# Kernel optimization log

Measured on AMD Instinct MI355X. Metric: run time of the kernel, lower is better.

## Reference

```python
import jax, jax.numpy as jnp
import numpy as np


def setup_inputs() -> dict:
    key = jax.random.key(0)
    k1, k2, k3, k4 = jax.random.split(key, 4)
    B, C, H, W = 8, 64, 64, 64
    Ck = C // 8  # query/key channels
    x = jax.random.normal(k1, (B, C, H, W), dtype=jnp.float32)
    # 1x1 conv1d weights (bias=False); spectral norm only rescales the weight,
    # so plain matrices are math-equivalent at a given parameter value.
    wq = jax.random.normal(k2, (Ck, C), dtype=jnp.float32) * (1.0 / np.sqrt(C))
    wk = jax.random.normal(k3, (Ck, C), dtype=jnp.float32) * (1.0 / np.sqrt(C))
    wv = jax.random.normal(k4, (C, C), dtype=jnp.float32) * (1.0 / np.sqrt(C))
    gamma = jnp.array([0.5], dtype=jnp.float32)  # nonzero so attention path is exercised
    return {"x": x, "wq": wq, "wk": wk, "wv": wv, "gamma": gamma}


def reference(x, wq, wk, wv, gamma):
    B, C, H, W = x.shape
    xf = x.reshape(B, C, H * W)                      # [B, C, N]
    f = jnp.einsum('kc,bcn->bkn', wq, xf)            # [B, C/8, N]
    g = jnp.einsum('kc,bcn->bkn', wk, xf)            # [B, C/8, N]
    h = jnp.einsum('oc,bcn->bon', wv, xf)            # [B, C,   N]
    scores = jnp.einsum('bkn,bkm->bnm', f, g)        # f^T g, [B, N, N]
    beta = jax.nn.softmax(scores, axis=1)            # softmax over dim=1 (rows), as in torch
    o = jnp.einsum('bcn,bnm->bcm', h, beta)          # [B, C, N]
    out = gamma[0] * o + xf
    return out.reshape(B, C, H, W)
```

## Files before the change

### kernel.cpp

```cpp
#include <hip/hip_runtime.h>
#include <hip/hip_bf16.h>

typedef __bf16 bf16x8 __attribute__((ext_vector_type(8)));
typedef float f32x4 __attribute__((ext_vector_type(4)));
typedef float f32x16 __attribute__((ext_vector_type(16)));
typedef unsigned int uint2v __attribute__((ext_vector_type(2)));

#define MFMA16 __builtin_amdgcn_mfma_f32_16x16x32_bf16
#define MFMA32 __builtin_amdgcn_mfma_f32_32x32x16_bf16

__device__ __forceinline__ unsigned short f2b(float f) {
  unsigned int u = __float_as_uint(f);
  u += 0x7FFFu + ((u >> 16) & 1u);
  return (unsigned short)(u >> 16);
}

__device__ __forceinline__ float b2f(unsigned short s) {
  return __uint_as_float(((unsigned)s) << 16);
}

union U128 {
  uint4 u;
  unsigned short s[8];
  bf16x8 b;
};

union BPack {
  __hip_bfloat162 h2;
  unsigned u;
};

__device__ __forceinline__ unsigned packbf(float a, float b) {
  BPack p;
  p.h2 = __float22bfloat162_rn(make_float2(a, b));
  return p.u;
}

__global__ __launch_bounds__(256, 2) void proj_kernel(
    const float* __restrict__ x, const float* __restrict__ wq,
    const float* __restrict__ wk, const float* __restrict__ wv_w,
    unsigned short* __restrict__ f_t, unsigned short* __restrict__ g_t,
    unsigned short* __restrict__ h_out) {
  __shared__ unsigned short xT[64 * 64];
  __shared__ unsigned short wT[96 * 72];

  const int tid = (int)threadIdx.x;
  const int wvp = tid >> 6;
  const int lane = tid & 63;
  const int b = (int)blockIdx.x & 7;
  const int n0 = ((int)blockIdx.x >> 3) << 6;

  {
    const float* xb = x + ((size_t)b << 18) + n0 + lane;
    const int c0 = wvp * 16;
    float xv[16];
#pragma unroll
    for (int cc = 0; cc < 16; ++cc) xv[cc] = xb[(size_t)(c0 + cc) << 12];
#pragma unroll
    for (int p = 0; p < 4; ++p) {
      const int c = c0 + 4 * p;
      uint2 d;
      d.x = packbf(xv[4 * p + 0], xv[4 * p + 1]);
      d.y = packbf(xv[4 * p + 2], xv[4 * p + 3]);
      const int g = c >> 3;
      const int idx = lane * 64 + (((g ^ (lane & 7)) << 3) | (((c >> 2) & 1) << 2));
      *(uint2*)&xT[idx] = d;
    }
  }
#pragma unroll
  for (int i = 0; i < 20; ++i) {
    const int idx = i * 256 + tid;
    const float wval = (idx < 512) ? wq[idx] * 1.44269504f
                     : (idx < 1024) ? wk[idx - 512]
                                    : wv_w[idx - 1024];
    wT[(idx >> 6) * 72 + (idx & 63)] = f2b(wval);
  }
  __syncthreads();

  const int t = lane & 15, q = lane >> 4;
  const int nloc = wvp * 16 + t;
  U128 Bf[2];
#pragma unroll
  for (int kp = 0; kp < 2; ++kp) {
    const int g = kp * 4 + q;
    Bf[kp].u = *(const uint4*)&xT[nloc * 64 + ((g ^ (nloc & 7)) << 3)];
  }
  const int nabs = n0 + nloc;
#pragma unroll
  for (int rt = 0; rt < 5; ++rt) {
    f32x4 acc = {0.f, 0.f, 0.f, 0.f};
#pragma unroll
    for (int kp = 0; kp < 2; ++kp) {
      U128 Af;
      Af.u = *(const uint4*)&wT[(rt * 16 + t) * 72 + ((kp * 4 + q) << 3)];
      acc = MFMA16(Af.b, Bf[kp].b, acc, 0, 0, 0);
    }
#pragma unroll
    for (int reg = 0; reg < 4; ++reg) {
      const int r = rt * 16 + 4 * q + reg;
      const unsigned short v = f2b(acc[reg]);
      if (r < 8)
        f_t[((size_t)((b << 12) + nabs) << 3) + r] = v;
      else if (r < 16)
        g_t[((size_t)((b << 12) + nabs) << 3) + (r - 8)] = v;
      else
        h_out[((size_t)b << 18) + ((size_t)(nabs >> 3) << 9) +
              ((r - 16) << 3) + (nabs & 7)] = v;
    }
  }
}

__global__ __launch_bounds__(256, 4) void attn_kernel(
    const unsigned short* __restrict__ f_t, const unsigned short* __restrict__ g_t,
    const unsigned short* __restrict__ h, const float* __restrict__ x,
    const float* __restrict__ gamma, float* __restrict__ out) {
  __shared__ unsigned short Opart[4][32][66];
  __shared__ float lred[4][32];
  __shared__ float lsum[32];

  const int tid = (int)threadIdx.x;
  const int wave = tid >> 6;
  const int lane = tid & 63;
  const int ml = lane & 31;
  const int hh = lane >> 5;

  const int b = (int)blockIdx.x & 7;
  const int m32 = ((int)blockIdx.x >> 3) << 5;

  const unsigned short* fb = f_t + ((size_t)b << 15);
  const unsigned short* hb = h + ((size_t)b << 18);

  U128 G;
  G.u = make_uint4(0u, 0u, 0u, 0u);
  if (hh == 0) G.u = *(const uint4*)(g_t + ((size_t)((b << 12) + m32 + ml) << 3));

  f32x16 O0 = {}, O1 = {};
  float lp = 0.f;

  const int nbase = wave << 10;

  const unsigned short* fp = fb + ((size_t)(nbase + ml) << 3);
  const unsigned short* hp = hb + ((nbase >> 3) << 9) + (hh << 9) + (ml << 3);

  U128 F0, F1, Ha0[4], Ha1[4];
  F0.u = *(const uint4*)(fp);
  Ha0[0].u = *(const uint4*)(hp);
  Ha0[1].u = *(const uint4*)(hp + 256);
  Ha0[2].u = *(const uint4*)(hp + 1024);
  Ha0[3].u = *(const uint4*)(hp + 1280);

  auto body = [&](const U128& Fv, const U128* Hv) {
    const f32x16 z = {};
    f32x16 S = MFMA32(Fv.b, G.b, z, 0, 0, 0);
    float e[16];
#pragma unroll
    for (int r = 0; r < 16; ++r) e[r] = __builtin_amdgcn_exp2f(S[r]);
    lp += (((e[0] + e[1]) + (e[2] + e[3])) + ((e[4] + e[5]) + (e[6] + e[7]))) +
          (((e[8] + e[9]) + (e[10] + e[11])) + ((e[12] + e[13]) + (e[14] + e[15])));
#pragma unroll
    for (int kt = 0; kt < 2; ++kt) {
      const unsigned A0 = packbf(e[8 * kt + 0], e[8 * kt + 1]);
      const unsigned A1 = packbf(e[8 * kt + 2], e[8 * kt + 3]);
      const unsigned B0 = packbf(e[8 * kt + 4], e[8 * kt + 5]);
      const unsigned B1 = packbf(e[8 * kt + 6], e[8 * kt + 7]);
      const uint2v r0 = __builtin_amdgcn_permlane32_swap(A0, B0, false, false);
      const uint2v r1 = __builtin_amdgcn_permlane32_swap(A1, B1, false, false);
      U128 P;
      P.u.x = r0[0];
      P.u.y = r1[0];
      P.u.z = r0[1];
      P.u.w = r1[1];
      O0 = MFMA32(Hv[2 * kt + 0].b, P.b, O0, 0, 0, 0);
      O1 = MFMA32(Hv[2 * kt + 1].b, P.b, O1, 0, 0, 0);
    }
  };

#pragma unroll 1
  for (int it2 = 0; it2 < 15; ++it2) {
    F1.u = *(const uint4*)(fp + 256);
    Ha1[0].u = *(const uint4*)(hp + 2048);
    Ha1[1].u = *(const uint4*)(hp + 2304);
    Ha1[2].u = *(const uint4*)(hp + 3072);
    Ha1[3].u = *(const uint4*)(hp + 3328);
    body(F0, Ha0);
    F0.u = *(const uint4*)(fp + 512);
    Ha0[0].u = *(const uint4*)(hp + 4096);
    Ha0[1].u = *(const uint4*)(hp + 4352);
    Ha0[2].u = *(const uint4*)(hp + 5120);
    Ha0[3].u = *(const uint4*)(hp + 5376);
    body(F1, Ha1);
    fp += 512;
    hp += 4096;
  }
  F1.u = *(const uint4*)(fp + 256);
  Ha1[0].u = *(const uint4*)(hp + 2048);
  Ha1[1].u = *(const uint4*)(hp + 2304);
  Ha1[2].u = *(const uint4*)(hp + 3072);
  Ha1[3].u = *(const uint4*)(hp + 3328);
  body(F0, Ha0);
  body(F1, Ha1);

  lp += __shfl_xor(lp, 32, 64);
  if (hh == 0) lred[wave][ml] = lp;
#pragma unroll
  for (int r = 0; r < 8; ++r) {
    const int c0 = ((2 * r) & 3) + 8 * (r >> 1) + 4 * hh;
    *(unsigned*)&Opart[wave][ml][c0] = packbf(O0[2 * r], O0[2 * r + 1]);
    *(unsigned*)&Opart[wave][ml][c0 + 32] = packbf(O1[2 * r], O1[2 * r + 1]);
  }
  __syncthreads();
  if (tid < 32)
    lsum[tid] = (lred[0][tid] + lred[1][tid]) + (lred[2][tid] + lred[3][tid]);
  __syncthreads();

  const int c = tid >> 2;
  const int m0l = (tid & 3) << 3;
  const float gam = gamma[0];
  float a[8];
#pragma unroll
  for (int j = 0; j < 8; ++j) a[j] = 0.f;
#pragma unroll
  for (int w = 0; w < 4; ++w)
#pragma unroll
    for (int j = 0; j < 8; ++j) a[j] += b2f(Opart[w][m0l + j][c]);

  const f32x4 l0 = *(const f32x4*)&lsum[m0l];
  const f32x4 l1 = *(const f32x4*)&lsum[m0l + 4];
  const size_t oi = (((size_t)b * 64 + c) << 12) + m32 + m0l;
  f32x4 xo0 = *(const f32x4*)(x + oi);
  f32x4 xo1 = *(const f32x4*)(x + oi + 4);
#pragma unroll
  for (int j = 0; j < 4; ++j) {
    xo0[j] += gam / l0[j] * a[j];
    xo1[j] += gam / l1[j] * a[j + 4];
  }
  *(f32x4*)(out + oi) = xo0;
  *(f32x4*)(out + oi + 4) = xo1;
}

extern "C" void kernel_launch(void* const* d_in, const int* in_sizes, int n_in,
                              void* d_out, int out_size, void* d_ws, size_t ws_size,
                              hipStream_t stream) {
  (void)in_sizes; (void)n_in; (void)out_size; (void)ws_size;
  const float* x = (const float*)d_in[0];
  const float* wq = (const float*)d_in[1];
  const float* wk = (const float*)d_in[2];
  const float* wv = (const float*)d_in[3];
  const float* gamma = (const float*)d_in[4];
  float* out = (float*)d_out;

  unsigned short* f_t = (unsigned short*)d_ws;
  unsigned short* g_t = f_t + (size_t)8 * 4096 * 8;
  unsigned short* h = g_t + (size_t)8 * 4096 * 8;

  proj_kernel<<<512, 256, 0, stream>>>(x, wq, wk, wv, f_t, g_t, h);
  attn_kernel<<<1024, 256, 0, stream>>>(f_t, g_t, h, x, gamma, out);
}
```

Measured before the change: 104.4 us.

## Software-pipeline score MFMA one step ahead and raise MFMA wave priority

Restructures the attention inner loop so the score MFMA for the next key tile is issued while the exp2 and packing of the current tile proceed, using double-buffered score accumulators and F prefetch two steps ahead. It also wraps MFMA issues in s_setprio to favour matrix instructions across waves. This aims to hide MFMA latency behind the transcendental and permute work, at the cost of extra live f32x16 registers that may pressure occupancy at 4 blocks per CU.

After: 133.4 us. +27.8%, slower.

```diff
diff --git a/kernel.cpp b/kernel.cpp
--- a/kernel.cpp
+++ b/kernel.cpp
@@ -136,25 +136,36 @@
 
   f32x16 O0 = {}, O1 = {};
   float lp = 0.f;
+  const f32x16 ZC = {};
 
   const int nbase = wave << 10;
 
   const unsigned short* fp = fb + ((size_t)(nbase + ml) << 3);
   const unsigned short* hp = hb + ((nbase >> 3) << 9) + (hh << 9) + (ml << 3);
 
-  U128 F0, F1, Ha0[4], Ha1[4];
-  F0.u = *(const uint4*)(fp);
-  Ha0[0].u = *(const uint4*)(hp);
-  Ha0[1].u = *(const uint4*)(hp + 256);
-  Ha0[2].u = *(const uint4*)(hp + 1024);
-  Ha0[3].u = *(const uint4*)(hp + 1280);
-
-  auto body = [&](const U128& Fv, const U128* Hv) {
-    const f32x16 z = {};
-    f32x16 S = MFMA32(Fv.b, G.b, z, 0, 0, 0);
+  U128 F_A, F_B, F_C, F_D, Ha_e[4], Ha_o[4];
+  f32x16 S_e, S_o;
+
+  F_A.u = *(const uint4*)(fp);
+  F_B.u = *(const uint4*)(fp + 256);
+  Ha_e[0].u = *(const uint4*)(hp);
+  Ha_e[1].u = *(const uint4*)(hp + 256);
+  Ha_e[2].u = *(const uint4*)(hp + 1024);
+  Ha_e[3].u = *(const uint4*)(hp + 1280);
+  __builtin_amdgcn_s_setprio(1);
+  S_e = MFMA32(F_A.b, G.b, ZC, 0, 0, 0);
+  __builtin_amdgcn_s_setprio(0);
+
+  auto body = [&](const f32x16& Sc, const U128* Hv, const U128& Fn, f32x16& Sn,
+                  bool produce) {
     float e[16];
 #pragma unroll
-    for (int r = 0; r < 16; ++r) e[r] = __builtin_amdgcn_exp2f(S[r]);
+    for (int r = 0; r < 16; ++r) e[r] = __builtin_amdgcn_exp2f(Sc[r]);
+    if (produce) {
+      __builtin_amdgcn_s_setprio(1);
+      Sn = MFMA32(Fn.b, G.b, ZC, 0, 0, 0);
+      __builtin_amdgcn_s_setprio(0);
+    }
     lp += (((e[0] + e[1]) + (e[2] + e[3])) + ((e[4] + e[5]) + (e[6] + e[7]))) +
           (((e[8] + e[9]) + (e[10] + e[11])) + ((e[12] + e[13]) + (e[14] + e[15])));
 #pragma unroll
@@ -170,35 +181,60 @@
       P.u.y = r1[0];
       P.u.z = r0[1];
       P.u.w = r1[1];
+      __builtin_amdgcn_s_setprio(1);
       O0 = MFMA32(Hv[2 * kt + 0].b, P.b, O0, 0, 0, 0);
       O1 = MFMA32(Hv[2 * kt + 1].b, P.b, O1, 0, 0, 0);
+      __builtin_amdgcn_s_setprio(0);
     }
   };
 
 #pragma unroll 1
-  for (int it2 = 0; it2 < 15; ++it2) {
-    F1.u = *(const uint4*)(fp + 256);
-    Ha1[0].u = *(const uint4*)(hp + 2048);
-    Ha1[1].u = *(const uint4*)(hp + 2304);
-    Ha1[2].u = *(const uint4*)(hp + 3072);
-    Ha1[3].u = *(const uint4*)(hp + 3328);
-    body(F0, Ha0);
-    F0.u = *(const uint4*)(fp + 512);
-    Ha0[0].u = *(const uint4*)(hp + 4096);
-    Ha0[1].u = *(const uint4*)(hp + 4352);
-    Ha0[2].u = *(const uint4*)(hp + 5120);
-    Ha0[3].u = *(const uint4*)(hp + 5376);
-    body(F1, Ha1);
-    fp += 512;
-    hp += 4096;
-  }
-  F1.u = *(const uint4*)(fp + 256);
-  Ha1[0].u = *(const uint4*)(hp + 2048);
-  Ha1[1].u = *(const uint4*)(hp + 2304);
-  Ha1[2].u = *(const uint4*)(hp + 3072);
-  Ha1[3].u = *(const uint4*)(hp + 3328);
-  body(F0, Ha0);
-  body(F1, Ha1);
+  for (int j = 0; j < 7; ++j) {
+    F_C.u = *(const uint4*)(fp + 512);
+    F_D.u = *(const uint4*)(fp + 768);
+    Ha_o[0].u = *(const uint4*)(hp + 2048);
+    Ha_o[1].u = *(const uint4*)(hp + 2304);
+    Ha_o[2].u = *(const uint4*)(hp + 3072);
+    Ha_o[3].u = *(const uint4*)(hp + 3328);
+    body(S_e, Ha_e, F_B, S_o, true);
+    Ha_e[0].u = *(const uint4*)(hp + 4096);
+    Ha_e[1].u = *(const uint4*)(hp + 4352);
+    Ha_e[2].u = *(const uint4*)(hp + 5120);
+    Ha_e[3].u = *(const uint4*)(hp + 5376);
+    body(S_o, Ha_o, F_C, S_e, true);
+    F_A.u = *(const uint4*)(fp + 1024);
+    F_B.u = *(const uint4*)(fp + 1280);
+    Ha_o[0].u = *(const uint4*)(hp + 6144);
+    Ha_o[1].u = *(const uint4*)(hp + 6400);
+    Ha_o[2].u = *(const uint4*)(hp + 7168);
+    Ha_o[3].u = *(const uint4*)(hp + 7424);
+    body(S_e, Ha_e, F_D, S_o, true);
+    Ha_e[0].u = *(const uint4*)(hp + 8192);
+    Ha_e[1].u = *(const uint4*)(hp + 8448);
+    Ha_e[2].u = *(const uint4*)(hp + 9216);
+    Ha_e[3].u = *(const uint4*)(hp + 9472);
+    body(S_o, Ha_o, F_A, S_e, true);
+    fp += 1024;
+    hp += 8192;
+  }
+  F_C.u = *(const uint4*)(fp + 512);
+  F_D.u = *(const uint4*)(fp + 768);
+  Ha_o[0].u = *(const uint4*)(hp + 2048);
+  Ha_o[1].u = *(const uint4*)(hp + 2304);
+  Ha_o[2].u = *(const uint4*)(hp + 3072);
+  Ha_o[3].u = *(const uint4*)(hp + 3328);
+  body(S_e, Ha_e, F_B, S_o, true);
+  Ha_e[0].u = *(const uint4*)(hp + 4096);
+  Ha_e[1].u = *(const uint4*)(hp + 4352);
+  Ha_e[2].u = *(const uint4*)(hp + 5120);
+  Ha_e[3].u = *(const uint4*)(hp + 5376);
+  body(S_o, Ha_o, F_C, S_e, true);
+  Ha_o[0].u = *(const uint4*)(hp + 6144);
+  Ha_o[1].u = *(const uint4*)(hp + 6400);
+  Ha_o[2].u = *(const uint4*)(hp + 7168);
+  Ha_o[3].u = *(const uint4*)(hp + 7424);
+  body(S_e, Ha_e, F_D, S_o, true);
+  body(S_o, Ha_o, F_D, S_o, false);
 
   lp += __shfl_xor(lp, 32, 64);
   if (hh == 0) lred[wave][ml] = lp;
```
